# Kernel optimization log

Hardware: AMD Instinct MI355X
Metric: run time of the kernel (lower is better)

## Reference

```python
import jax, jax.numpy as jnp
import numpy as np

B, C, D, H = 2, 1024, 1024, 16
DH = D // H
EPS = 1e-8


def setup_inputs() -> dict:
    key = jax.random.key(0)
    ks = jax.random.split(key, 12)
    s = 0.02
    return {
        "x": jax.random.normal(ks[0], (B, C, D), dtype=jnp.float32),
        "rms_w": jnp.ones((C, D), dtype=jnp.float32),
        "rms_b": jnp.zeros((C, D), dtype=jnp.float32),
        "Wqkv": jax.random.normal(ks[1], (3 * D, D), dtype=jnp.float32) * s,
        "Wout": jax.random.normal(ks[2], (D, D), dtype=jnp.float32) * s,
        "bout": jnp.zeros((D,), dtype=jnp.float32),
        "Wf": jax.random.normal(ks[3], (D, D), dtype=jnp.float32) * s,
        "bf": jnp.zeros((D,), dtype=jnp.float32),
        "Ww": jax.random.normal(ks[4], (D, D), dtype=jnp.float32) * s,
        "bw": jnp.zeros((D,), dtype=jnp.float32),
        "Wv": jax.random.normal(ks[5], (D, D), dtype=jnp.float32) * s,
        "bv": jnp.zeros((D,), dtype=jnp.float32),
        "beta": jnp.ones((1,), dtype=jnp.float32),
    }


def _rope_cos_sin(C, dh):
    # faithful to source: theta = 10000 ** (-2*(i-1)/dh), i in [0, dh//2)
    i = jnp.arange(dh // 2, dtype=jnp.float32)
    theta = 10000.0 ** (-2.0 * (i - 1.0) / dh)            # [dh//2]
    ang = jnp.arange(C, dtype=jnp.float32)[:, None] * theta  # [C, dh//2]
    return jnp.cos(ang), jnp.sin(ang)


def _rotate(t, cos, sin):
    # equivalent to einsum('bhci,cij->bhcj', t, R) with the source R
    ev, od = t[..., 0::2], t[..., 1::2]          # [B,H,C,dh//2]
    out_ev = ev * cos + od * sin
    out_od = -ev * sin + od * cos
    return jnp.stack([out_ev, out_od], axis=-1).reshape(t.shape)


def _rmsnorm(x, w, b):
    rms = jnp.sqrt(jnp.mean(x * x, axis=-1, keepdims=True) + EPS)
    return w * (x / rms) + b


def _attention(x, Wqkv, Wout, bout):
    qkv = x @ Wqkv.T                               # [B,C,3D]
    q, k, v = jnp.split(qkv, 3, axis=-1)
    def heads(t):
        return t.reshape(B, C, H, DH).transpose(0, 2, 1, 3)  # [B,H,C,dh]
    q, k, v = heads(q), heads(k), heads(v)
    cos, sin = _rope_cos_sin(C, DH)
    qr = _rotate(q, cos, sin)
    kr = _rotate(k, cos, sin)
    scale = 1.0 / jnp.sqrt(jnp.float32(DH))
    num = jnp.exp(jnp.einsum('bhid,bhjd->bhij', qr, kr) * scale)
    den = jnp.sum(jnp.exp(jnp.einsum('bhid,bhjd->bhij', q, k) * scale),
                  axis=-1, keepdims=True)
    attn = num / den
    mask = jnp.tril(jnp.ones((C, C), dtype=bool))
    attn = jnp.where(mask[None, None], attn, 0.0)
    y = attn @ v                                   # [B,H,C,dh]
    y = y.transpose(0, 2, 1, 3).reshape(B, C, D)
    return y @ Wout.T + bout


def _ffn(x, Wf, bf, Ww, bw, Wv, bv, beta):
    h = x @ Wf.T + bf
    wx = h @ Ww.T + bw
    swish = wx * jax.nn.sigmoid(beta * wx)
    return swish * (h @ Wv.T + bv)


def reference(x, rms_w, rms_b, Wqkv, Wout, bout, Wf, bf, Ww, bw, Wv, bv, beta):
    # dropout p is identity in eval mode
    x = _rmsnorm(x, rms_w, rms_b)
    x = x + _attention(x, Wqkv, Wout, bout)
    x = _rmsnorm(x, rms_w, rms_b)   # same shared RMSNorm module applied twice
    x = x + _ffn(x, Wf, bf, Ww, bw, Wv, bv, beta)
    return x
```

## Files before the change

kernel.cpp:

```cpp
#include <hip/hip_runtime.h>
#include <math.h>

#define B_ 2
#define C_ 1024
#define D_ 1024
#define H_ 16
#define DH_ 64
#define EPSF 1e-8f

typedef __bf16 bf16;
typedef __attribute__((ext_vector_type(4))) __bf16 bf16x4;
typedef __attribute__((ext_vector_type(8))) __bf16 bf16x8;
typedef __attribute__((ext_vector_type(4))) float f32x4;

__device__ inline f32x4 mfma16(bf16x8 a, bf16x8 b, f32x4 c) {
  return __builtin_amdgcn_mfma_f32_16x16x32_bf16(a, b, c, 0, 0, 0);
}

__device__ inline void async16(const bf16* g, bf16* l) {
  __builtin_amdgcn_global_load_lds((const __attribute__((address_space(1))) void*)g,
                                   (__attribute__((address_space(3))) void*)l, 16, 0, 0);
}

#define S_BARRIER() asm volatile("s_barrier" ::: "memory")
#define S_VMCNT(N) asm volatile("s_waitcnt vmcnt(" #N ")" ::: "memory")

__device__ inline float rope_theta(float i) {
  return exp2f(-13.287712379549449f * (2.0f * (i - 1.0f) * (1.0f / 64.0f)));
}

__global__ __launch_bounds__(256) void cvt_rms_kernel(const float* __restrict__ wqkv,
                                                      const float* __restrict__ wout,
                                                      const float* __restrict__ wf,
                                                      const float* __restrict__ www,
                                                      const float* __restrict__ wv,
                                                      bf16* __restrict__ wdst,
                                                      const float* __restrict__ x,
                                                      const float* __restrict__ rw,
                                                      const float* __restrict__ rb,
                                                      bf16* __restrict__ xout) {
  __shared__ float red[4];
  int t = threadIdx.x;
  if (blockIdx.x < 7 * 1024) {
    int seg = blockIdx.x >> 10;
    int local = (blockIdx.x & 1023) * 1024 + t * 4;
    const float* src = seg < 3 ? wqkv + (size_t)seg * (D_ * D_)
                     : seg == 3 ? wout : seg == 4 ? wf : seg == 5 ? www : wv;
    float4 v = *(const float4*)(src + local);
    bf16x4 o;
    o[0] = (bf16)v.x; o[1] = (bf16)v.y; o[2] = (bf16)v.z; o[3] = (bf16)v.w;
    *(bf16x4*)(wdst + (size_t)seg * (D_ * D_) + local) = o;
    return;
  }
  int row = blockIdx.x - 7 * 1024;
  int c = row & (C_ - 1);
  float4 xv = *(const float4*)(x + (size_t)row * D_ + t * 4);
  float ss = xv.x * xv.x + xv.y * xv.y + xv.z * xv.z + xv.w * xv.w;
#pragma unroll
  for (int m = 1; m < 64; m <<= 1) ss += __shfl_xor(ss, m, 64);
  if ((t & 63) == 0) red[t >> 6] = ss;
  __syncthreads();
  float tot = red[0] + red[1] + red[2] + red[3];
  float inv = rsqrtf(tot * (1.0f / D_) + EPSF);
  float4 wv4 = *(const float4*)(rw + (size_t)c * D_ + t * 4);
  float4 bv4 = *(const float4*)(rb + (size_t)c * D_ + t * 4);
  bf16x4 ov;
  ov[0] = (bf16)(wv4.x * (xv.x * inv) + bv4.x);
  ov[1] = (bf16)(wv4.y * (xv.y * inv) + bv4.y);
  ov[2] = (bf16)(wv4.z * (xv.z * inv) + bv4.z);
  ov[3] = (bf16)(wv4.w * (xv.w * inv) + bv4.w);
  *(bf16x4*)(xout + (size_t)row * D_ + t * 4) = ov;
}

__global__ __launch_bounds__(256) void rmsnorm_bf16_kernel(const bf16* __restrict__ x,
                                                           const float* __restrict__ w,
                                                           const float* __restrict__ b,
                                                           bf16* __restrict__ out) {
  int row = blockIdx.x;
  int c = row & (C_ - 1);
  int t = threadIdx.x;
  bf16x4 xv = *(const bf16x4*)(x + (size_t)row * D_ + t * 4);
  float f0 = (float)xv[0], f1 = (float)xv[1], f2 = (float)xv[2], f3 = (float)xv[3];
  float ss = f0 * f0 + f1 * f1 + f2 * f2 + f3 * f3;
#pragma unroll
  for (int m = 1; m < 64; m <<= 1) ss += __shfl_xor(ss, m, 64);
  __shared__ float red[4];
  if ((t & 63) == 0) red[t >> 6] = ss;
  __syncthreads();
  float tot = red[0] + red[1] + red[2] + red[3];
  float inv = rsqrtf(tot * (1.0f / D_) + EPSF);
  float4 wv = *(const float4*)(w + (size_t)c * D_ + t * 4);
  float4 bv = *(const float4*)(b + (size_t)c * D_ + t * 4);
  bf16x4 ov;
  ov[0] = (bf16)(wv.x * (f0 * inv) + bv.x);
  ov[1] = (bf16)(wv.y * (f1 * inv) + bv.y);
  ov[2] = (bf16)(wv.z * (f2 * inv) + bv.z);
  ov[3] = (bf16)(wv.w * (f3 * inv) + bv.w);
  *(bf16x4*)(out + (size_t)row * D_ + t * 4) = ov;
}

template <int BMt, int BNt>
__global__ __launch_bounds__(256) void gemm_lds(const bf16* __restrict__ A,
                                                const bf16* __restrict__ W,
                                                const float* __restrict__ bias,
                                                const bf16* __restrict__ R,
                                                bf16* __restrict__ Cout,
                                                int M, int N, int K) {
  constexpr int BK = 128;
  constexpr int MT = BMt / 32;
  constexpr int NT = BNt / 32;
  __shared__ bf16 sa[2][BMt * BK];
  __shared__ bf16 sb[2][BNt * BK];
  int t = threadIdx.x, l = t & 63, w = t >> 6;
  int m0 = blockIdx.y * BMt;
  int n0 = blockIdx.x * BNt;
  int wm = (w >> 1) * (BMt / 2), wn = (w & 1) * (BNt / 2);
  int lm = l & 15, lq = l >> 4;
  int swz = lm & 7;
  f32x4 acc[MT][NT] = {};

  auto stage = [&](int buf, int k0) {
#pragma unroll
    for (int p = 0; p < BMt / 16; ++p) {
      int lin = p * 256 + t;
      int r = lin >> 4, cc = (lin & 15) ^ (r & 7);
      async16(A + (size_t)(m0 + r) * K + k0 + cc * 8, &sa[buf][lin * 8]);
    }
#pragma unroll
    for (int p = 0; p < BNt / 16; ++p) {
      int lin = p * 256 + t;
      int r = lin >> 4, cc = (lin & 15) ^ (r & 7);
      async16(W + (size_t)(n0 + r) * K + k0 + cc * 8, &sb[buf][lin * 8]);
    }
  };

  int NKi = K / BK;
  stage(0, 0);
  int cur = 0;
  for (int i = 0; i < NKi; ++i) {
    if (i + 1 < NKi) {
      stage(cur ^ 1, (i + 1) * BK);
      S_VMCNT(8);
    } else {
      S_VMCNT(0);
    }
    S_BARRIER();
#pragma unroll
    for (int hh = 0; hh < 4; ++hh) {
      bf16x8 af[MT], bfr[NT];
#pragma unroll
      for (int mt = 0; mt < MT; ++mt)
        af[mt] = *(const bf16x8*)(&sa[cur][0] + (wm + mt * 16 + lm) * BK +
                                  ((((hh << 2) | lq) ^ swz) << 3));
#pragma unroll
      for (int nt = 0; nt < NT; ++nt)
        bfr[nt] = *(const bf16x8*)(&sb[cur][0] + (wn + nt * 16 + lm) * BK +
                                   ((((hh << 2) | lq) ^ swz) << 3));
#pragma unroll
      for (int mt = 0; mt < MT; ++mt)
#pragma unroll
        for (int nt = 0; nt < NT; ++nt)
          acc[mt][nt] = mfma16(af[mt], bfr[nt], acc[mt][nt]);
    }
    S_BARRIER();
    cur ^= 1;
  }
#pragma unroll
  for (int mt = 0; mt < MT; ++mt)
#pragma unroll
    for (int nt = 0; nt < NT; ++nt) {
      int col = n0 + wn + nt * 16 + lm;
      float bb = bias ? bias[col] : 0.0f;
#pragma unroll
      for (int r = 0; r < 4; ++r) {
        int row = m0 + wm + mt * 16 + lq * 4 + r;
        float v = acc[mt][nt][r] + bb;
        if (R) v += (float)R[(size_t)row * N + col];
        Cout[(size_t)row * N + col] = (bf16)v;
      }
    }
}

__global__ __launch_bounds__(256) void gemm_qkv_kernel(const bf16* __restrict__ A,
                                                       const bf16* __restrict__ W,
                                                       bf16* __restrict__ qkv,
                                                       bf16* __restrict__ vt) {
  constexpr int BK = 64;
  constexpr int BMt = 128, BNt = 64, MT = 4, NT = 2;
  const int N = 3 * D_, K = D_;
  __shared__ bf16 sa[2][BMt * BK];
  __shared__ bf16 sb[2][BNt * BK];
  int t = threadIdx.x, l = t & 63, w = t >> 6;
  int m0 = blockIdx.y * BMt;
  int n0 = blockIdx.x * BNt;
  int wm = (w >> 1) * 64, wn = (w & 1) * 32;
  int lm = l & 15, lq = l >> 4;
  int swz = lm & 7;
  f32x4 acc[MT][NT] = {};

  auto stage = [&](int buf, int k0) {
#pragma unroll
    for (int p = 0; p < 4; ++p) {
      int lin = p * 256 + t;
      int r = lin >> 3, cc = (lin & 7) ^ (r & 7);
      async16(A + (size_t)(m0 + r) * K + k0 + cc * 8, &sa[buf][lin * 8]);
    }
#pragma unroll
    for (int p = 0; p < 2; ++p) {
      int lin = p * 256 + t;
      int r = lin >> 3, cc = (lin & 7) ^ (r & 7);
      async16(W + (size_t)(n0 + r) * K + k0 + cc * 8, &sb[buf][lin * 8]);
    }
  };

  int NKi = K / BK;
  stage(0, 0);
  int cur = 0;
  for (int i = 0; i < NKi; ++i) {
    if (i + 1 < NKi) {
      stage(cur ^ 1, (i + 1) * BK);
      S_VMCNT(6);
    } else {
      S_VMCNT(0);
    }
    S_BARRIER();
    bf16x8 af[MT][2], bfr[NT][2];
#pragma unroll
    for (int mt = 0; mt < MT; ++mt) {
      const bf16* base = &sa[cur][0] + (wm + mt * 16 + lm) * BK;
      af[mt][0] = *(const bf16x8*)(base + ((lq ^ swz) << 3));
      af[mt][1] = *(const bf16x8*)(base + (((4 | lq) ^ swz) << 3));
    }
#pragma unroll
    for (int nt = 0; nt < NT; ++nt) {
      const bf16* base = &sb[cur][0] + (wn + nt * 16 + lm) * BK;
      bfr[nt][0] = *(const bf16x8*)(base + ((lq ^ swz) << 3));
      bfr[nt][1] = *(const bf16x8*)(base + (((4 | lq) ^ swz) << 3));
    }
#pragma unroll
    for (int mt = 0; mt < MT; ++mt)
#pragma unroll
      for (int nt = 0; nt < NT; ++nt) {
        acc[mt][nt] = mfma16(af[mt][0], bfr[nt][0], acc[mt][nt]);
        acc[mt][nt] = mfma16(af[mt][1], bfr[nt][1], acc[mt][nt]);
      }
    S_BARRIER();
    cur ^= 1;
  }
  if (n0 < 2 * D_) {
#pragma unroll
    for (int mt = 0; mt < MT; ++mt)
#pragma unroll
      for (int nt = 0; nt < NT; ++nt) {
        int col = n0 + wn + nt * 16 + lm;
#pragma unroll
        for (int r = 0; r < 4; ++r) {
          int row = m0 + wm + mt * 16 + lq * 4 + r;
          qkv[(size_t)row * N + col] = (bf16)acc[mt][nt][r];
        }
      }
  } else {
    bf16* tv = &sa[0][0];
#pragma unroll
    for (int mt = 0; mt < MT; ++mt)
#pragma unroll
      for (int nt = 0; nt < NT; ++nt) {
        int dh = wn + nt * 16 + lm;
#pragma unroll
        for (int r = 0; r < 4; ++r)
          tv[dh * 136 + wm + mt * 16 + lq * 4 + r] = (bf16)acc[mt][nt][r];
      }
    __syncthreads();
    int h = (n0 - 2 * D_) >> 6;
    int bb = m0 >> 10;
    int mloc = m0 & 1023;
    size_t vbase = (size_t)((bb * H_ + h) * DH_) * C_;
#pragma unroll
    for (int p = 0; p < 4; ++p) {
      int lin = p * 256 + t;
      int dh = lin >> 4;
      int mm = (lin & 15) * 8;
      *(int4*)(vt + vbase + (size_t)dh * C_ + mloc + mm) = *(int4*)(tv + dh * 136 + mm);
    }
  }
}

__global__ __launch_bounds__(256) void gemm_ffn_kernel(const bf16* __restrict__ A,
                                                       const bf16* __restrict__ Ww,
                                                       const bf16* __restrict__ Wv,
                                                       const float* __restrict__ bw,
                                                       const float* __restrict__ bv,
                                                       const bf16* __restrict__ x3,
                                                       const float* __restrict__ beta_p,
                                                       float* __restrict__ out) {
  constexpr int BK = 64;
  __shared__ bf16 sa[2][64 * BK];
  __shared__ bf16 sb1[2][64 * BK];
  __shared__ bf16 sb2[2][64 * BK];
  int t = threadIdx.x, l = t & 63, w = t >> 6;
  int m0 = blockIdx.y * 64, n0 = blockIdx.x * 64;
  int wm = (w >> 1) * 32, wn = (w & 1) * 32;
  int lm = l & 15, lq = l >> 4;
  int swz = lm & 7;
  float beta = beta_p[0];
  f32x4 acc1[2][2] = {}, acc2[2][2] = {};

  auto stage = [&](int buf, int k0) {
#pragma unroll
    for (int p = 0; p < 2; ++p) {
      int lin = p * 256 + t;
      int r = lin >> 3, cc = (lin & 7) ^ (r & 7);
      async16(A + (size_t)(m0 + r) * D_ + k0 + cc * 8, &sa[buf][lin * 8]);
      async16(Ww + (size_t)(n0 + r) * D_ + k0 + cc * 8, &sb1[buf][lin * 8]);
      async16(Wv + (size_t)(n0 + r) * D_ + k0 + cc * 8, &sb2[buf][lin * 8]);
    }
  };

  int NKi = D_ / BK;
  stage(0, 0);
  int cur = 0;
  for (int i = 0; i < NKi; ++i) {
    if (i + 1 < NKi) {
      stage(cur ^ 1, (i + 1) * BK);
      S_VMCNT(6);
    } else {
      S_VMCNT(0);
    }
    S_BARRIER();
    bf16x8 af[2][2], b1f[2][2], b2f[2][2];
#pragma unroll
    for (int mt = 0; mt < 2; ++mt) {
      const bf16* base = &sa[cur][0] + (wm + mt * 16 + lm) * BK;
      af[mt][0] = *(const bf16x8*)(base + ((lq ^ swz) << 3));
      af[mt][1] = *(const bf16x8*)(base + (((4 | lq) ^ swz) << 3));
    }
#pragma unroll
    for (int nt = 0; nt < 2; ++nt) {
      const bf16* base1 = &sb1[cur][0] + (wn + nt * 16 + lm) * BK;
      const bf16* base2 = &sb2[cur][0] + (wn + nt * 16 + lm) * BK;
      b1f[nt][0] = *(const bf16x8*)(base1 + ((lq ^ swz) << 3));
      b1f[nt][1] = *(const bf16x8*)(base1 + (((4 | lq) ^ swz) << 3));
      b2f[nt][0] = *(const bf16x8*)(base2 + ((lq ^ swz) << 3));
      b2f[nt][1] = *(const bf16x8*)(base2 + (((4 | lq) ^ swz) << 3));
    }
#pragma unroll
    for (int mt = 0; mt < 2; ++mt)
#pragma unroll
      for (int nt = 0; nt < 2; ++nt) {
        acc1[mt][nt] = mfma16(af[mt][0], b1f[nt][0], acc1[mt][nt]);
        acc1[mt][nt] = mfma16(af[mt][1], b1f[nt][1], acc1[mt][nt]);
        acc2[mt][nt] = mfma16(af[mt][0], b2f[nt][0], acc2[mt][nt]);
        acc2[mt][nt] = mfma16(af[mt][1], b2f[nt][1], acc2[mt][nt]);
      }
    S_BARRIER();
    cur ^= 1;
  }
#pragma unroll
  for (int mt = 0; mt < 2; ++mt)
#pragma unroll
    for (int nt = 0; nt < 2; ++nt) {
      int col = n0 + wn + nt * 16 + lm;
      float bbw = bw[col], bbv = bv[col];
#pragma unroll
      for (int r = 0; r < 4; ++r) {
        int row = m0 + wm + mt * 16 + lq * 4 + r;
        float z = acc1[mt][nt][r] + bbw;
        float g = acc2[mt][nt][r] + bbv;
        float sw_ = z / (1.0f + __expf(-beta * z));
        out[(size_t)row * D_ + col] = (float)x3[(size_t)row * D_ + col] + sw_ * g;
      }
    }
}

__global__ __launch_bounds__(256) void attn_kernel(const bf16* __restrict__ qkv,
                                                   const bf16* __restrict__ vt,
                                                   bf16* __restrict__ y) {
  __shared__ bf16 sk[64 * 72];
  __shared__ bf16 skr[64 * 72];
  __shared__ bf16 sv[64 * 72];
  __shared__ bf16 pl[4][16 * 72];
  int t = threadIdx.x, l = t & 63, w = t >> 6;
  int blk = blockIdx.x;
  int idx = blk & 255;
  int it = (blk < 256) ? (idx >> 5) : (15 - (idx >> 5));
  int r5 = idx & 31;
  int b = r5 >> 4;
  int h = r5 & 15;
  int i_base = it * 64 + w * 16;
  int lm = l & 15, lq = l >> 4;
  const float scale = 0.125f;

  size_t hq = (size_t)h * DH_;
  size_t qrow = (size_t)(b * C_ + i_base + lm) * (3 * D_) + hq;
  bf16x8 qp[2], qrf[2];
  float cq = (float)(i_base + lm);
#pragma unroll
  for (int kk = 0; kk < 2; ++kk) {
    qp[kk] = *(const bf16x8*)(qkv + qrow + kk * 32 + lq * 8);
#pragma unroll
    for (int j = 0; j < 4; ++j) {
      float ip = (float)(kk * 16 + lq * 4 + j);
      float ang = cq * rope_theta(ip);
      float sv_, cv_;
      __sincosf(ang, &sv_, &cv_);
      float qe = (float)qp[kk][2 * j], qo = (float)qp[kk][2 * j + 1];
      qrf[kk][2 * j] = (bf16)(qe * cv_ + qo * sv_);
      qrf[kk][2 * j + 1] = (bf16)(qo * cv_ - qe * sv_);
    }
  }

  float den[4] = {0.f, 0.f, 0.f, 0.f};
  f32x4 yacc[4] = {};
  int i_max = i_base + 15;
  size_t kbase = (size_t)(b * C_) * (3 * D_) + D_ + hq;
  size_t vtbase = (size_t)((b * H_ + h) * DH_) * C_;
  int sr = t >> 3;
  int sc = (t & 7) * 8;
  float th0 = rope_theta((float)((sc >> 1) + 0));
  float th1 = rope_theta((float)((sc >> 1) + 1));
  float th2 = rope_theta((float)((sc >> 1) + 2));
  float th3 = rope_theta((float)((sc >> 1) + 3));

  int4 pk0, pk1, pv0, pv1, rk0, rk1;
#define FETCH_TILE(J0)                                                          \
  pk0 = *(const int4*)(qkv + kbase + (size_t)((J0) + sr) * (3 * D_) + sc);      \
  pk1 = *(const int4*)(qkv + kbase + (size_t)((J0) + 32 + sr) * (3 * D_) + sc); \
  pv0 = *(const int4*)(vt + vtbase + (size_t)sr * C_ + (J0) + sc);              \
  pv1 = *(const int4*)(vt + vtbase + (size_t)(32 + sr) * C_ + (J0) + sc);

#define ROTP(KV, RV, P)                                       \
  {                                                           \
    float e = (float)KV[2 * P], o = (float)KV[2 * P + 1];     \
    RV[2 * P] = (bf16)(e * c_ + o * s_);                      \
    RV[2 * P + 1] = (bf16)(o * c_ - e * s_);                  \
  }
#define ROTATE(J0)                                            \
  {                                                           \
    bf16x8 k0 = *(bf16x8*)&pk0, k1 = *(bf16x8*)&pk1;          \
    bf16x8 r0, r1;                                            \
    float jA = (float)((J0) + sr), jB = (float)((J0) + 32 + sr); \
    float s_, c_;                                             \
    __sincosf(jA * th0, &s_, &c_); ROTP(k0, r0, 0)            \
    __sincosf(jA * th1, &s_, &c_); ROTP(k0, r0, 1)            \
    __sincosf(jA * th2, &s_, &c_); ROTP(k0, r0, 2)            \
    __sincosf(jA * th3, &s_, &c_); ROTP(k0, r0, 3)            \
    __sincosf(jB * th0, &s_, &c_); ROTP(k1, r1, 0)            \
    __sincosf(jB * th1, &s_, &c_); ROTP(k1, r1, 1)            \
    __sincosf(jB * th2, &s_, &c_); ROTP(k1, r1, 2)            \
    __sincosf(jB * th3, &s_, &c_); ROTP(k1, r1, 3)            \
    rk0 = *(int4*)&r0;                                        \
    rk1 = *(int4*)&r1;                                        \
  }

  FETCH_TILE(0)
  ROTATE(0)

  for (int j0 = 0; j0 < C_; j0 += 64) {
    __syncthreads();
    *(int4*)(sk + sr * 72 + sc) = pk0;
    *(int4*)(sk + (32 + sr) * 72 + sc) = pk1;
    *(int4*)(skr + sr * 72 + sc) = rk0;
    *(int4*)(skr + (32 + sr) * 72 + sc) = rk1;
    *(int4*)(sv + sr * 72 + sc) = pv0;
    *(int4*)(sv + (32 + sr) * 72 + sc) = pv1;
    __syncthreads();
    if (j0 + 64 < C_) {
      FETCH_TILE(j0 + 64)
    }
#pragma unroll
    for (int js = 0; js < 64; js += 16) {
      bf16x8 kf0 = *(const bf16x8*)(sk + (js + lm) * 72 + lq * 8);
      bf16x8 kf1 = *(const bf16x8*)(sk + (js + lm) * 72 + 32 + lq * 8);
      f32x4 s = {0.f, 0.f, 0.f, 0.f};
      s = mfma16(qp[0], kf0, s);
      s = mfma16(qp[1], kf1, s);
#pragma unroll
      for (int r = 0; r < 4; ++r) den[r] += __expf(s[r] * scale);
    }
    if (j0 <= i_max) {
#pragma unroll
      for (int js = 0; js < 64; js += 16) {
        bf16x8 kf0 = *(const bf16x8*)(skr + (js + lm) * 72 + lq * 8);
        bf16x8 kf1 = *(const bf16x8*)(skr + (js + lm) * 72 + 32 + lq * 8);
        f32x4 s = {0.f, 0.f, 0.f, 0.f};
        s = mfma16(qrf[0], kf0, s);
        s = mfma16(qrf[1], kf1, s);
#pragma unroll
        for (int r = 0; r < 4; ++r) {
          int jg = j0 + js + lm;
          int ig = i_base + lq * 4 + r;
          float p = (jg <= ig) ? __expf(s[r] * scale) : 0.0f;
          pl[w][(lq * 4 + r) * 72 + js + lm] = (bf16)p;
        }
      }
      __builtin_amdgcn_wave_barrier();
      bf16x8 pf0 = *(const bf16x8*)(pl[w] + lm * 72 + lq * 8);
      bf16x8 pf1 = *(const bf16x8*)(pl[w] + lm * 72 + 32 + lq * 8);
#pragma unroll
      for (int tt = 0; tt < 4; ++tt) {
        bf16x8 vf0 = *(const bf16x8*)(sv + (tt * 16 + lm) * 72 + lq * 8);
        bf16x8 vf1 = *(const bf16x8*)(sv + (tt * 16 + lm) * 72 + 32 + lq * 8);
        yacc[tt] = mfma16(pf0, vf0, mfma16(pf1, vf1, yacc[tt]));
      }
      __builtin_amdgcn_wave_barrier();
    }
    if (j0 + 64 < C_) {
      ROTATE(j0 + 64)
    }
  }
#undef FETCH_TILE
#undef ROTATE
#undef ROTP
  float inv[4];
#pragma unroll
  for (int r = 0; r < 4; ++r) {
    float d = den[r];
    d += __shfl_xor(d, 1, 64);
    d += __shfl_xor(d, 2, 64);
    d += __shfl_xor(d, 4, 64);
    d += __shfl_xor(d, 8, 64);
    inv[r] = 1.0f / d;
  }
#pragma unroll
  for (int tt = 0; tt < 4; ++tt)
#pragma unroll
    for (int r = 0; r < 4; ++r) {
      int ig = i_base + lq * 4 + r;
      y[(size_t)(b * C_ + ig) * D_ + hq + tt * 16 + lm] = (bf16)(yacc[tt][r] * inv[r]);
    }
}

extern "C" void kernel_launch(void* const* d_in, const int* in_sizes, int n_in,
                              void* d_out, int out_size, void* d_ws, size_t ws_size,
                              hipStream_t stream) {
  const float* x = (const float*)d_in[0];
  const float* rms_w = (const float*)d_in[1];
  const float* rms_b = (const float*)d_in[2];
  const float* Wqkv = (const float*)d_in[3];
  const float* Wout = (const float*)d_in[4];
  const float* bout = (const float*)d_in[5];
  const float* Wf = (const float*)d_in[6];
  const float* bfp = (const float*)d_in[7];
  const float* Ww = (const float*)d_in[8];
  const float* bw = (const float*)d_in[9];
  const float* Wv = (const float*)d_in[10];
  const float* bv = (const float*)d_in[11];
  const float* beta = (const float*)d_in[12];
  float* out = (float*)d_out;

  bf16* ws = (bf16*)d_ws;
  const size_t DD = (size_t)D_ * D_;
  const size_t MC = (size_t)B_ * C_;
  bf16* wb = ws;
  bf16* x1 = ws + 7 * DD;
  bf16* qkv = ws + 9 * DD;
  bf16* vt = ws + 15 * DD;
  bf16* x2 = ws + 17 * DD;
  bf16* x3 = ws + 19 * DD;
  bf16* hbuf = ws + 21 * DD;
  bf16* y = (bf16*)d_out;

  cvt_rms_kernel<<<7 * 1024 + MC, 256, 0, stream>>>(Wqkv, Wout, Wf, Ww, Wv, wb, x, rms_w,
                                                    rms_b, x1);
  gemm_qkv_kernel<<<dim3(3 * D_ / 64, MC / 128), 256, 0, stream>>>(x1, wb, qkv, vt);
  attn_kernel<<<B_ * H_ * 16, 256, 0, stream>>>(qkv, vt, y);
  gemm_lds<64, 64><<<dim3(D_ / 64, MC / 64), 256, 0, stream>>>(
      y, wb + 3 * DD, bout, x1, x2, MC, D_, D_);
  rmsnorm_bf16_kernel<<<MC, 256, 0, stream>>>(x2, rms_w, rms_b, x3);
  gemm_lds<64, 64><<<dim3(D_ / 64, MC / 64), 256, 0, stream>>>(
      x3, wb + 4 * DD, bfp, nullptr, hbuf, MC, D_, D_);
  gemm_ffn_kernel<<<dim3(D_ / 64, MC / 64), 256, 0, stream>>>(
      hbuf, wb + 5 * DD, wb + 6 * DD, bw, bv, x3, beta, out);
}
```

Before: 203.9 us.

## Split attention into separate denominator and causal PV kernels

The fused attention kernel is split in two. A new den_kernel computes the non-causal softmax denominator over all keys, with each block covering half the key range, and writes per-half partial sums to workspace. attn_pv_kernel then does the rotated causal numerator and PV product with 32-row query tiles and 128 threads, stops at the causal limit, and reads the two partial denominators. This spreads the uneven causal work across more blocks and removes the full-length denominator loop from the PV path. The cost is an extra launch, reloading Q and K in both kernels, and a small workspace round-trip.

```diff
diff --git a/kernel.cpp b/kernel.cpp
--- a/kernel.cpp
+++ b/kernel.cpp
@@ -372,46 +372,111 @@
     }
 }
 
-__global__ __launch_bounds__(256) void attn_kernel(const bf16* __restrict__ qkv,
-                                                   const bf16* __restrict__ vt,
-                                                   bf16* __restrict__ y) {
-  __shared__ bf16 sk[64 * 72];
+__global__ __launch_bounds__(256) void den_kernel(const bf16* __restrict__ qkv,
+                                                  float* __restrict__ dpart) {
+  __shared__ bf16 sk[2][64 * 72];
+  int t = threadIdx.x, l = t & 63, w = t >> 6;
+  int blk = blockIdx.x;
+  int it = blk & 15;
+  int jh = (blk >> 4) & 1;
+  int r5 = blk >> 5;
+  int b = r5 >> 4, h = r5 & 15;
+  int i_base = it * 64 + w * 16;
+  int lm = l & 15, lq = l >> 4;
+  const float scale = 0.125f;
+
+  size_t hq = (size_t)h * DH_;
+  size_t qrow = (size_t)(b * C_ + i_base + lm) * (3 * D_) + hq;
+  bf16x8 qp[2];
+  qp[0] = *(const bf16x8*)(qkv + qrow + lq * 8);
+  qp[1] = *(const bf16x8*)(qkv + qrow + 32 + lq * 8);
+
+  float den[4] = {0.f, 0.f, 0.f, 0.f};
+  size_t kbase = (size_t)(b * C_) * (3 * D_) + D_ + hq;
+  int jbase = jh * 512;
+  int sr = t >> 3;
+  int sc = (t & 7) * 8;
+
+  int4 pk0, pk1;
+#define DFETCH(J0)                                                              \
+  pk0 = *(const int4*)(qkv + kbase + (size_t)((J0) + sr) * (3 * D_) + sc);      \
+  pk1 = *(const int4*)(qkv + kbase + (size_t)((J0) + 32 + sr) * (3 * D_) + sc);
+
+  DFETCH(jbase)
+  for (int jt = 0; jt < 8; ++jt) {
+    int bu = jt & 1;
+    *(int4*)(&sk[bu][0] + sr * 72 + sc) = pk0;
+    *(int4*)(&sk[bu][0] + (32 + sr) * 72 + sc) = pk1;
+    __syncthreads();
+    if (jt + 1 < 8) {
+      DFETCH(jbase + (jt + 1) * 64)
+    }
+#pragma unroll
+    for (int js = 0; js < 64; js += 16) {
+      bf16x8 kf0 = *(const bf16x8*)(&sk[bu][0] + (js + lm) * 72 + lq * 8);
+      bf16x8 kf1 = *(const bf16x8*)(&sk[bu][0] + (js + lm) * 72 + 32 + lq * 8);
+      f32x4 s = {0.f, 0.f, 0.f, 0.f};
+      s = mfma16(qp[0], kf0, s);
+      s = mfma16(qp[1], kf1, s);
+#pragma unroll
+      for (int r = 0; r < 4; ++r) den[r] += __expf(s[r] * scale);
+    }
+  }
+#undef DFETCH
+#pragma unroll
+  for (int r = 0; r < 4; ++r) {
+    float d = den[r];
+    d += __shfl_xor(d, 1, 64);
+    d += __shfl_xor(d, 2, 64);
+    d += __shfl_xor(d, 4, 64);
+    d += __shfl_xor(d, 8, 64);
+    if (lm == 0)
+      dpart[(size_t)jh * (B_ * H_ * C_) + (size_t)(b * H_ + h) * C_ + i_base + lq * 4 + r] = d;
+  }
+}
+
+__global__ __launch_bounds__(128) void attn_pv_kernel(const bf16* __restrict__ qkv,
+                                                      const bf16* __restrict__ vt,
+                                                      const float* __restrict__ dpart,
+                                                      bf16* __restrict__ y) {
   __shared__ bf16 skr[64 * 72];
   __shared__ bf16 sv[64 * 72];
-  __shared__ bf16 pl[4][16 * 72];
+  __shared__ bf16 pl[2][16 * 72];
   int t = threadIdx.x, l = t & 63, w = t >> 6;
   int blk = blockIdx.x;
   int idx = blk & 255;
-  int it = (blk < 256) ? (idx >> 5) : (15 - (idx >> 5));
+  int qq = blk >> 8;
+  int u = idx >> 5;
+  int it32 = (qq == 0) ? u : (qq == 1) ? (31 - u) : (qq == 2) ? (8 + u) : (23 - u);
   int r5 = idx & 31;
   int b = r5 >> 4;
   int h = r5 & 15;
-  int i_base = it * 64 + w * 16;
+  int i_base = it32 * 32 + w * 16;
   int lm = l & 15, lq = l >> 4;
   const float scale = 0.125f;
 
   size_t hq = (size_t)h * DH_;
   size_t qrow = (size_t)(b * C_ + i_base + lm) * (3 * D_) + hq;
-  bf16x8 qp[2], qrf[2];
+  bf16x8 qrf[2];
   float cq = (float)(i_base + lm);
 #pragma unroll
   for (int kk = 0; kk < 2; ++kk) {
-    qp[kk] = *(const bf16x8*)(qkv + qrow + kk * 32 + lq * 8);
+    bf16x8 qp = *(const bf16x8*)(qkv + qrow + kk * 32 + lq * 8);
 #pragma unroll
     for (int j = 0; j < 4; ++j) {
       float ip = (float)(kk * 16 + lq * 4 + j);
       float ang = cq * rope_theta(ip);
       float sv_, cv_;
       __sincosf(ang, &sv_, &cv_);
-      float qe = (float)qp[kk][2 * j], qo = (float)qp[kk][2 * j + 1];
+      float qe = (float)qp[2 * j], qo = (float)qp[2 * j + 1];
       qrf[kk][2 * j] = (bf16)(qe * cv_ + qo * sv_);
       qrf[kk][2 * j + 1] = (bf16)(qo * cv_ - qe * sv_);
     }
   }
 
-  float den[4] = {0.f, 0.f, 0.f, 0.f};
   f32x4 yacc[4] = {};
   int i_max = i_base + 15;
+  int ntile = ((it32 * 32 + 31) >> 6) + 1;
   size_t kbase = (size_t)(b * C_) * (3 * D_) + D_ + hq;
   size_t vtbase = (size_t)((b * H_ + h) * DH_) * C_;
   int sr = t >> 3;
@@ -421,105 +486,99 @@
   float th2 = rope_theta((float)((sc >> 1) + 2));
   float th3 = rope_theta((float)((sc >> 1) + 3));
 
-  int4 pk0, pk1, pv0, pv1, rk0, rk1;
-#define FETCH_TILE(J0)                                                          \
+  int4 pk0, pk1, pk2, pk3, pv0, pv1, pv2, pv3, rk0, rk1, rk2, rk3;
+#define PFETCH(J0)                                                              \
   pk0 = *(const int4*)(qkv + kbase + (size_t)((J0) + sr) * (3 * D_) + sc);      \
-  pk1 = *(const int4*)(qkv + kbase + (size_t)((J0) + 32 + sr) * (3 * D_) + sc); \
+  pk1 = *(const int4*)(qkv + kbase + (size_t)((J0) + 16 + sr) * (3 * D_) + sc); \
+  pk2 = *(const int4*)(qkv + kbase + (size_t)((J0) + 32 + sr) * (3 * D_) + sc); \
+  pk3 = *(const int4*)(qkv + kbase + (size_t)((J0) + 48 + sr) * (3 * D_) + sc); \
   pv0 = *(const int4*)(vt + vtbase + (size_t)sr * C_ + (J0) + sc);              \
-  pv1 = *(const int4*)(vt + vtbase + (size_t)(32 + sr) * C_ + (J0) + sc);
-
-#define ROTP(KV, RV, P)                                       \
+  pv1 = *(const int4*)(vt + vtbase + (size_t)(16 + sr) * C_ + (J0) + sc);       \
+  pv2 = *(const int4*)(vt + vtbase + (size_t)(32 + sr) * C_ + (J0) + sc);       \
+  pv3 = *(const int4*)(vt + vtbase + (size_t)(48 + sr) * C_ + (J0) + sc);
+
+#define ROTP1(KV, RV, P)                                      \
   {                                                           \
     float e = (float)KV[2 * P], o = (float)KV[2 * P + 1];     \
     RV[2 * P] = (bf16)(e * c_ + o * s_);                      \
     RV[2 * P + 1] = (bf16)(o * c_ - e * s_);                  \
   }
-#define ROTATE(J0)                                            \
+#define ROTK(PKI, RKI, JROW)                                  \
   {                                                           \
-    bf16x8 k0 = *(bf16x8*)&pk0, k1 = *(bf16x8*)&pk1;          \
-    bf16x8 r0, r1;                                            \
-    float jA = (float)((J0) + sr), jB = (float)((J0) + 32 + sr); \
+    bf16x8 kk_ = *(bf16x8*)&PKI;                              \
+    bf16x8 rr_;                                               \
+    float jA = (float)(JROW);                                 \
     float s_, c_;                                             \
-    __sincosf(jA * th0, &s_, &c_); ROTP(k0, r0, 0)            \
-    __sincosf(jA * th1, &s_, &c_); ROTP(k0, r0, 1)            \
-    __sincosf(jA * th2, &s_, &c_); ROTP(k0, r0, 2)            \
-    __sincosf(jA * th3, &s_, &c_); ROTP(k0, r0, 3)            \
-    __sincosf(jB * th0, &s_, &c_); ROTP(k1, r1, 0)            \
-    __sincosf(jB * th1, &s_, &c_); ROTP(k1, r1, 1)            \
-    __sincosf(jB * th2, &s_, &c_); ROTP(k1, r1, 2)            \
-    __sincosf(jB * th3, &s_, &c_); ROTP(k1, r1, 3)            \
-    rk0 = *(int4*)&r0;                                        \
-    rk1 = *(int4*)&r1;                                        \
-  }
-
-  FETCH_TILE(0)
-  ROTATE(0)
-
-  for (int j0 = 0; j0 < C_; j0 += 64) {
+    __sincosf(jA * th0, &s_, &c_); ROTP1(kk_, rr_, 0)         \
+    __sincosf(jA * th1, &s_, &c_); ROTP1(kk_, rr_, 1)         \
+    __sincosf(jA * th2, &s_, &c_); ROTP1(kk_, rr_, 2)         \
+    __sincosf(jA * th3, &s_, &c_); ROTP1(kk_, rr_, 3)         \
+    RKI = *(int4*)&rr_;                                       \
+  }
+#define PROTATE(J0)                    \
+  ROTK(pk0, rk0, (J0) + sr)            \
+  ROTK(pk1, rk1, (J0) + 16 + sr)       \
+  ROTK(pk2, rk2, (J0) + 32 + sr)       \
+  ROTK(pk3, rk3, (J0) + 48 + sr)
+
+  PFETCH(0)
+  PROTATE(0)
+
+  for (int jt = 0; jt < ntile; ++jt) {
+    int j0 = jt * 64;
     __syncthreads();
-    *(int4*)(sk + sr * 72 + sc) = pk0;
-    *(int4*)(sk + (32 + sr) * 72 + sc) = pk1;
     *(int4*)(skr + sr * 72 + sc) = rk0;
-    *(int4*)(skr + (32 + sr) * 72 + sc) = rk1;
+    *(int4*)(skr + (16 + sr) * 72 + sc) = rk1;
+    *(int4*)(skr + (32 + sr) * 72 + sc) = rk2;
+    *(int4*)(skr + (48 + sr) * 72 + sc) = rk3;
     *(int4*)(sv + sr * 72 + sc) = pv0;
-    *(int4*)(sv + (32 + sr) * 72 + sc) = pv1;
+    *(int4*)(sv + (16 + sr) * 72 + sc) = pv1;
+    *(int4*)(sv + (32 + sr) * 72 + sc) = pv2;
+    *(int4*)(sv + (48 + sr) * 72 + sc) = pv3;
     __syncthreads();
-    if (j0 + 64 < C_) {
-      FETCH_TILE(j0 + 64)
+    if (jt + 1 < ntile) {
+      PFETCH(j0 + 64)
     }
 #pragma unroll
     for (int js = 0; js < 64; js += 16) {
-      bf16x8 kf0 = *(const bf16x8*)(sk + (js + lm) * 72 + lq * 8);
-      bf16x8 kf1 = *(const bf16x8*)(sk + (js + lm) * 72 + 32 + lq * 8);
+      bf16x8 kf0 = *(const bf16x8*)(skr + (js + lm) * 72 + lq * 8);
+      bf16x8 kf1 = *(const bf16x8*)(skr + (js + lm) * 72 + 32 + lq * 8);
       f32x4 s = {0.f, 0.f, 0.f, 0.f};
-      s = mfma16(qp[0], kf0, s);
-      s = mfma16(qp[1], kf1, s);
-#pragma unroll
-      for (int r = 0; r < 4; ++r) den[r] += __expf(s[r] * scale);
-    }
-    if (j0 <= i_max) {
-#pragma unroll
-      for (int js = 0; js < 64; js += 16) {
-        bf16x8 kf0 = *(const bf16x8*)(skr + (js + lm) * 72 + lq * 8);
-        bf16x8 kf1 = *(const bf16x8*)(skr + (js + lm) * 72 + 32 + lq * 8);
-        f32x4 s = {0.f, 0.f, 0.f, 0.f};
-        s = mfma16(qrf[0], kf0, s);
-        s = mfma16(qrf[1], kf1, s);
-#pragma unroll
-        for (int r = 0; r < 4; ++r) {
-          int jg = j0 + js + lm;
-          int ig = i_base + lq * 4 + r;
-          float p = (jg <= ig) ? __expf(s[r] * scale) : 0.0f;
-          pl[w][(lq * 4 + r) * 72 + js + lm] = (bf16)p;
-        }
+      s = mfma16(qrf[0], kf0, s);
+      s = mfma16(qrf[1], kf1, s);
+#pragma unroll
+      for (int r = 0; r < 4; ++r) {
+        int jg = j0 + js + lm;
+        int ig = i_base + lq * 4 + r;
+        float p = (jg <= ig) ? __expf(s[r] * scale) : 0.0f;
+        pl[w][(lq * 4 + r) * 72 + js + lm] = (bf16)p;
       }
-      __builtin_amdgcn_wave_barrier();
-      bf16x8 pf0 = *(const bf16x8*)(pl[w] + lm * 72 + lq * 8);
-      bf16x8 pf1 = *(const bf16x8*)(pl[w] + lm * 72 + 32 + lq * 8);
-#pragma unroll
-      for (int tt = 0; tt < 4; ++tt) {
-        bf16x8 vf0 = *(const bf16x8*)(sv + (tt * 16 + lm) * 72 + lq * 8);
-        bf16x8 vf1 = *(const bf16x8*)(sv + (tt * 16 + lm) * 72 + 32 + lq * 8);
-        yacc[tt] = mfma16(pf0, vf0, mfma16(pf1, vf1, yacc[tt]));
-      }
-      __builtin_amdgcn_wave_barrier();
-    }
-    if (j0 + 64 < C_) {
-      ROTATE(j0 + 64)
-    }
-  }
-#undef FETCH_TILE
-#undef ROTATE
-#undef ROTP
+    }
+    __builtin_amdgcn_wave_barrier();
+    bf16x8 pf0 = *(const bf16x8*)(pl[w] + lm * 72 + lq * 8);
+    bf16x8 pf1 = *(const bf16x8*)(pl[w] + lm * 72 + 32 + lq * 8);
+#pragma unroll
+    for (int tt = 0; tt < 4; ++tt) {
+      bf16x8 vf0 = *(const bf16x8*)(sv + (tt * 16 + lm) * 72 + lq * 8);
+      bf16x8 vf1 = *(const bf16x8*)(sv + (tt * 16 + lm) * 72 + 32 + lq * 8);
+      yacc[tt] = mfma16(pf0, vf0, mfma16(pf1, vf1, yacc[tt]));
+    }
+    __builtin_amdgcn_wave_barrier();
+    if (jt + 1 < ntile) {
+      PROTATE(j0 + 64)
+    }
+  }
+#undef PFETCH
+#undef PROTATE
+#undef ROTK
+#undef ROTP1
+  const float* dp0 = dpart + (size_t)(b * H_ + h) * C_;
+  const float* dp1 = dpart + (size_t)(B_ * H_ * C_) + (size_t)(b * H_ + h) * C_;
   float inv[4];
 #pragma unroll
   for (int r = 0; r < 4; ++r) {
-    float d = den[r];
-    d += __shfl_xor(d, 1, 64);
-    d += __shfl_xor(d, 2, 64);
-    d += __shfl_xor(d, 4, 64);
-    d += __shfl_xor(d, 8, 64);
-    inv[r] = 1.0f / d;
+    int ig = i_base + lq * 4 + r;
+    inv[r] = 1.0f / (dp0[ig] + dp1[ig]);
   }
 #pragma unroll
   for (int tt = 0; tt < 4; ++tt)
@@ -558,12 +617,14 @@
   bf16* x2 = ws + 17 * DD;
   bf16* x3 = ws + 19 * DD;
   bf16* hbuf = ws + 21 * DD;
+  float* dpart = (float*)(ws + 23 * DD);
   bf16* y = (bf16*)d_out;
 
   cvt_rms_kernel<<<7 * 1024 + MC, 256, 0, stream>>>(Wqkv, Wout, Wf, Ww, Wv, wb, x, rms_w,
                                                     rms_b, x1);
   gemm_qkv_kernel<<<dim3(3 * D_ / 64, MC / 128), 256, 0, stream>>>(x1, wb, qkv, vt);
-  attn_kernel<<<B_ * H_ * 16, 256, 0, stream>>>(qkv, vt, y);
+  den_kernel<<<1024, 256, 0, stream>>>(qkv, dpart);
+  attn_pv_kernel<<<1024, 128, 0, stream>>>(qkv, vt, dpart, y);
   gemm_lds<64, 64><<<dim3(D_ / 64, MC / 64), 256, 0, stream>>>(
       y, wb + 3 * DD, bout, x1, x2, MC, D_, D_);
   rmsnorm_bf16_kernel<<<MC, 256, 0, stream>>>(x2, rms_w, rms_b, x3);
```

Result: no change. 206.6 us (+1.3%).
